# Kernel optimization log

Measured on AMD Instinct MI355X. Metric: run time of the kernel, lower is better.

## Reference

```python
import jax, jax.numpy as jnp
import numpy as np

T = 4      # num_step (also LSTM num_layers)
R = 64     # num_relation (= LSTM hidden size)
E = 1024   # num_entity
B = 128    # batch
IN = R + 2 * E  # LSTM input size


def _lstm_layer(x_seq, Wih, Whh, bih, bhh):
    # x_seq: [T, B, In]; torch gate order i, f, g, o
    Bsz = x_seq.shape[1]
    H = Whh.shape[1]
    pre = jnp.einsum('tbi,gi->tbg', x_seq, Wih) + bih + bhh  # [T,B,4H]

    def step(carry, z):
        h, c = carry
        z = z + h @ Whh.T
        i, f, g, o = jnp.split(z, 4, axis=-1)
        i, f, o = jax.nn.sigmoid(i), jax.nn.sigmoid(f), jax.nn.sigmoid(o)
        c = f * c + i * jnp.tanh(g)
        h = o * jnp.tanh(c)
        return (h, c), h

    init = (jnp.zeros((Bsz, H), x_seq.dtype), jnp.zeros((Bsz, H), x_seq.dtype))
    _, hs = jax.lax.scan(step, init, pre)
    return hs  # [T, B, H]


def setup_inputs() -> dict:
    key = jax.random.key(0)
    ks = jax.random.split(key, 12)
    s = 0.05
    inp = {
        'x': jax.random.uniform(ks[0], (B, IN), dtype=jnp.float32),
        'kb': jax.random.uniform(ks[1], (R, E, E), dtype=jnp.float32) * 0.01,
        # LSTM layer 0 (input dim IN)
        'Wih0': jax.random.normal(ks[2], (4 * R, IN), dtype=jnp.float32) * s,
        'Whh0': jax.random.normal(ks[3], (4 * R, R), dtype=jnp.float32) * s,
        'bih0': jnp.zeros((4 * R,), jnp.float32),
        'bhh0': jnp.zeros((4 * R,), jnp.float32),
        # LSTM layers 1..T-1 (input dim R)
        'Wih': jax.random.normal(ks[4], (T - 1, 4 * R, R), dtype=jnp.float32) * s,
        'Whh': jax.random.normal(ks[5], (T - 1, 4 * R, R), dtype=jnp.float32) * s,
        'bih': jnp.zeros((T - 1, 4 * R), jnp.float32),
        'bhh': jnp.zeros((T - 1, 4 * R), jnp.float32),
    }
    return inp


def reference(x, kb, Wih0, Whh0, bih0, bhh0, Wih, Whh, bih, bhh):
    # input to LSTM: x repeated T times -> [T, B, IN]
    seq = jnp.broadcast_to(x[None], (T,) + x.shape)
    hs = _lstm_layer(seq, Wih0, Whh0, bih0, bhh0)
    for l in range(T - 1):  # small fixed layer count
        hs = _lstm_layer(hs, Wih[l], Whh[l], bih[l], bhh[l])
    h = jax.nn.softmax(hs, axis=-1)  # [T, B, R] (first softmax)

    mem = [x[:, R:R + E]]  # memory[0] = head entity vector, [B, E]
    for i in range(T):
        h2 = jax.nn.softmax(h[i], axis=-1)  # double softmax, faithful to source
        # causal memory attention over steps k <= i
        att = jax.nn.softmax(jnp.einsum('kbr,br->bk', h[:i + 1], h[i]), axis=-1)  # [B, i+1]
        prev = jnp.einsum('bk,kbe->be', att, jnp.stack(mem))  # [B, E]
        # per-relation operator application: sum_r h2[b,r] * KB[r] @ prev[b]
        tmp = jnp.einsum('ref,bf->bre', kb, prev)  # [B, R, E]
        mem.append(jnp.einsum('br,bre->be', h2, tmp))

    tail = x[:, R + E:R + 2 * E]  # [B, E]
    score = jax.nn.sigmoid(-jnp.einsum('be,be->b', mem[-1], tail))[:, None]  # [B, 1]
    return score
```

## Files before the change

### kernel.cpp

```cpp
#include <hip/hip_runtime.h>
#include <cstdint>
#include <cstddef>

#define B_ 128
#define E_ 1024
#define R_ 64
#define T_ 4
#define IN_ 2112
#define G_ 256

typedef __attribute__((ext_vector_type(4))) float f32x4;
typedef __attribute__((ext_vector_type(8))) __bf16 bf16x8;

__device__ __forceinline__ unsigned short f2bf(float f) {
  unsigned int u = __float_as_uint(f);
  u += 0x7fffu + ((u >> 16) & 1u);
  return (unsigned short)(u >> 16);
}
__device__ __forceinline__ unsigned int pack2(float lo, float hi) {
  return (unsigned int)f2bf(lo) | ((unsigned int)f2bf(hi) << 16);
}
__device__ __forceinline__ float wred_sum(float v) {
#pragma unroll
  for (int m = 32; m > 0; m >>= 1) v += __shfl_xor(v, m, 64);
  return v;
}
__device__ __forceinline__ float wred_max(float v) {
#pragma unroll
  for (int m = 32; m > 0; m >>= 1) v = fmaxf(v, __shfl_xor(v, m, 64));
  return v;
}
__device__ __forceinline__ float sigmoidf_(float x) { return 1.f / (1.f + expf(-x)); }

__device__ __forceinline__ void gload_lds16(const void* g, void* l) {
  __builtin_amdgcn_global_load_lds(
      (const __attribute__((address_space(1))) unsigned int*)g,
      (__attribute__((address_space(3))) unsigned int*)l, 16, 0, 0);
}

__global__ __launch_bounds__(256) void head_kernel(
    const float* __restrict__ x, const float* __restrict__ kb,
    const float* __restrict__ Wih0, const float* __restrict__ Whh0,
    const float* __restrict__ bih0, const float* __restrict__ bhh0,
    const float* __restrict__ Wih, const float* __restrict__ Whh,
    const float* __restrict__ bih, const float* __restrict__ bhh,
    unsigned short* __restrict__ kb_bf,
    float* __restrict__ h2_out, float* __restrict__ att_out) {
  __shared__ float Wt[G_ * 65];
  __shared__ float xrow[IN_];
  __shared__ float hbuf[R_], cbuf[R_], zbuf[G_];
  __shared__ float hs_in[T_][R_], hs_out[T_][R_], hmat[T_][R_];
  const int tid = threadIdx.x;

  if (blockIdx.x >= 128) {
    const size_t base = (size_t)(blockIdx.x - 128) * 8192;
#pragma unroll
    for (int c = 0; c < 4; c++) {
      size_t o = base + (size_t)c * 2048 + (size_t)tid * 8;
      float4 v0 = *(const float4*)(kb + o);
      float4 v1 = *(const float4*)(kb + o + 4);
      uint4 u;
      u.x = pack2(v0.x, v0.y); u.y = pack2(v0.z, v0.w);
      u.z = pack2(v1.x, v1.y); u.w = pack2(v1.z, v1.w);
      *(uint4*)(kb_bf + o) = u;
    }
    return;
  }

  const int b = blockIdx.x;
  const int lane = tid & 63, wv = tid >> 6;

  for (int l = tid; l < IN_; l += 256) xrow[l] = x[b * IN_ + l];
  __syncthreads();
  float p0 = bih0[tid] + bhh0[tid];
  {
    const float* wr = Wih0 + (size_t)tid * IN_;
#pragma unroll 4
    for (int j = 0; j < IN_; j += 4) {
      float4 w = *(const float4*)(wr + j);
      p0 += xrow[j] * w.x + xrow[j + 1] * w.y + xrow[j + 2] * w.z + xrow[j + 3] * w.w;
    }
  }

  auto stage_w = [&](const float* src) {
    for (int l = tid; l < G_ * 16; l += 256) {
      int g = l >> 4, c4 = (l & 15) * 4;
      const float4 v = *(const float4*)(src + g * R_ + c4);
      float* dst = &Wt[g * 65 + c4];
      dst[0] = v.x; dst[1] = v.y; dst[2] = v.z; dst[3] = v.w;
    }
  };
  auto scan = [&](float* pret) {
    for (int t = 0; t < T_; t++) {
      float z = pret[t];
#pragma unroll
      for (int j = 0; j < R_; j++) z += hbuf[j] * Wt[tid * 65 + j];
      zbuf[tid] = z;
      __syncthreads();
      if (tid < R_) {
        float iv = sigmoidf_(zbuf[tid]);
        float fv = sigmoidf_(zbuf[R_ + tid]);
        float gv = tanhf(zbuf[2 * R_ + tid]);
        float ov = sigmoidf_(zbuf[3 * R_ + tid]);
        float c = fv * cbuf[tid] + iv * gv;
        cbuf[tid] = c;
        float h = ov * tanhf(c);
        hbuf[tid] = h;
        hs_out[t][tid] = h;
      }
      __syncthreads();
    }
  };

  float pret[T_];
#pragma unroll
  for (int t = 0; t < T_; t++) pret[t] = p0;
  stage_w(Whh0);
  if (tid < R_) { hbuf[tid] = 0.f; cbuf[tid] = 0.f; }
  __syncthreads();
  scan(pret);

  for (int l = 0; l < T_ - 1; l++) {
    hs_in[tid >> 6][tid & 63] = hs_out[tid >> 6][tid & 63];
    __syncthreads();
    stage_w(Wih + l * G_ * R_);
    __syncthreads();
    const float bsum = bih[l * G_ + tid] + bhh[l * G_ + tid];
    for (int t = 0; t < T_; t++) {
      float p = bsum;
#pragma unroll
      for (int j = 0; j < R_; j++) p += hs_in[t][j] * Wt[tid * 65 + j];
      pret[t] = p;
    }
    __syncthreads();
    stage_w(Whh + l * G_ * R_);
    if (tid < R_) { hbuf[tid] = 0.f; cbuf[tid] = 0.f; }
    __syncthreads();
    scan(pret);
  }

  {
    float v = hs_out[wv][lane];
    float mx = wred_max(v);
    float ev = expf(v - mx);
    float sm = wred_sum(ev);
    float hval = ev / sm;
    hmat[wv][lane] = hval;
    float mx2 = wred_max(hval);
    float e2 = expf(hval - mx2);
    float s2 = wred_sum(e2);
    h2_out[(wv * B_ + b) * R_ + lane] = e2 / s2;
    __syncthreads();
    float dots[T_];
    for (int k = 0; k <= wv; k++)
      dots[k] = wred_sum(hmat[k][lane] * hmat[wv][lane]);
    if (lane == 0) {
      float mx3 = dots[0];
      for (int k = 1; k <= wv; k++) mx3 = fmaxf(mx3, dots[k]);
      float ss = 0.f, es[T_];
      for (int k = 0; k <= wv; k++) { es[k] = expf(dots[k] - mx3); ss += es[k]; }
      for (int k = 0; k <= wv; k++) att_out[(wv * B_ + b) * 4 + k] = es[k] / ss;
    }
  }
}

__global__ __launch_bounds__(256) void prep0_kernel(
    const float* __restrict__ x, const float* __restrict__ att,
    unsigned short* __restrict__ prev_bf) {
  const int idx = blockIdx.x * 256 + threadIdx.x;
  const int b = idx >> 10, e = idx & 1023;
  float a0 = att[b * 4];
  prev_bf[idx] = f2bf(a0 * x[b * IN_ + R_ + e]);
}

__global__ __launch_bounds__(256) void gemm_bf_kernel(
    const unsigned short* __restrict__ Abf,
    const unsigned short* __restrict__ Kbf,
    float* __restrict__ part) {
  __shared__ unsigned short As[128 * 32];
  __shared__ unsigned short Bs[128 * 32];
  const int tid = threadIdx.x, wv = tid >> 6, lane = tid & 63;
  const int et = blockIdx.x, r = blockIdx.y;
  const int wm = (wv & 1) * 64, wn = (wv >> 1) * 64;
  const int fr = lane & 15, koff = (lane >> 4) * 8;

  const int srow = wv * 32 + (lane >> 2);
  const int scol = (lane & 3) * 8;
  const unsigned short* agp = Abf + (size_t)srow * 1024 + scol;
  const unsigned short* bgp = Kbf + (size_t)r * 1048576 + (size_t)(et * 128 + srow) * 1024 + scol;
  unsigned short* a_l0 = As + wv * 1024;
  unsigned short* a_l1 = As + wv * 1024 + 512;
  unsigned short* b_l0 = Bs + wv * 1024;
  unsigned short* b_l1 = Bs + wv * 1024 + 512;

  f32x4 acc[4][4];
#pragma unroll
  for (int mt = 0; mt < 4; mt++)
#pragma unroll
    for (int nt = 0; nt < 4; nt++)
#pragma unroll
      for (int q = 0; q < 4; q++) acc[mt][nt][q] = 0.f;

  for (int kk = 0; kk < 32; kk++) {
    gload_lds16(agp + kk * 32,             a_l0);
    gload_lds16(agp + kk * 32 + 16 * 1024, a_l1);
    gload_lds16(bgp + kk * 32,             b_l0);
    gload_lds16(bgp + kk * 32 + 16 * 1024, b_l1);
    __syncthreads();
    bf16x8 af[4], bfr[4];
#pragma unroll
    for (int mt = 0; mt < 4; mt++)
      af[mt] = *(const bf16x8*)(As + (wm + mt * 16 + fr) * 32 + koff);
#pragma unroll
    for (int nt = 0; nt < 4; nt++)
      bfr[nt] = *(const bf16x8*)(Bs + (wn + nt * 16 + fr) * 32 + koff);
#pragma unroll
    for (int mt = 0; mt < 4; mt++)
#pragma unroll
      for (int nt = 0; nt < 4; nt++)
        acc[mt][nt] = __builtin_amdgcn_mfma_f32_16x16x32_bf16(af[mt], bfr[nt], acc[mt][nt], 0, 0, 0);
    __syncthreads();
  }
  const int crow = (lane >> 4) * 4;
  float* pout = part + (size_t)r * 131072;
#pragma unroll
  for (int mt = 0; mt < 4; mt++)
#pragma unroll
    for (int nt = 0; nt < 4; nt++)
#pragma unroll
      for (int q = 0; q < 4; q++)
        pout[(wm + mt * 16 + crow + q) * 1024 + et * 128 + wn + nt * 16 + fr] = acc[mt][nt][q];
}

__global__ __launch_bounds__(256) void mid_kernel(
    const float* __restrict__ part, const float* __restrict__ h2,
    const float* __restrict__ att, const float* __restrict__ x,
    float* __restrict__ mem, unsigned short* __restrict__ prev_bf, int it) {
  const int idx = blockIdx.x * 256 + threadIdx.x;
  const int b = idx >> 10, e = idx & 1023;
  const float* h2row = h2 + (it * B_ + b) * R_;
  const float* pp = part + idx;
  float s = 0.f;
#pragma unroll 8
  for (int rr = 0; rr < 64; rr++) s += h2row[rr] * pp[(size_t)rr * 131072];
  mem[it * 131072 + idx] = s;
  if (it < 3) {
    const float* arow = att + ((it + 1) * B_ + b) * 4;
    float acc = arow[0] * x[b * IN_ + R_ + e];
    for (int k = 1; k <= it; k++) acc += arow[k] * mem[(k - 1) * 131072 + idx];
    acc += arow[it + 1] * s;
    prev_bf[idx] = f2bf(acc);
  }
}

__global__ __launch_bounds__(256) void prep_fp32_kernel(
    const float* __restrict__ x, const float* __restrict__ att,
    const float* __restrict__ mem, float* __restrict__ prev,
    float* __restrict__ newmem, int it) {
  const int idx = blockIdx.x * 256 + threadIdx.x;
  const int b = idx >> 10, e = idx & 1023;
  const float* arow = att + (it * B_ + b) * 4;
  float acc = arow[0] * x[b * IN_ + R_ + e];
  for (int k = 1; k <= it; k++)
    acc += arow[k] * mem[(k - 1) * (B_ * E_) + b * E_ + e];
  prev[idx] = acc;
  newmem[idx] = 0.f;
}

__global__ __launch_bounds__(256) void gemm_fp32_kernel(
    const float* __restrict__ prev, const float* __restrict__ h2,
    const float* __restrict__ kb, float* __restrict__ out) {
  __shared__ unsigned short As[128 * 40];
  __shared__ unsigned short Bs[128 * 40];
  __shared__ float h2s[128];
  const int tid = threadIdx.x;
  const int et = blockIdx.x;
  const int r = blockIdx.y;
  if (tid < 128) h2s[tid] = h2[tid * 64 + r];
  __syncthreads();
  const int row = tid >> 1;
  const int c0 = (tid & 1) * 16;
  const float hsc = h2s[row];
  const float* aptr = prev + row * 1024 + c0;
  const float* bptr = kb + (size_t)r * (1024u * 1024u) + (size_t)(et * 128 + row) * 1024 + c0;
  unsigned short* adst = As + row * 40 + c0;
  unsigned short* bdst = Bs + row * 40 + c0;
  const int wv = tid >> 6, lane = tid & 63;
  const int wm = (wv & 1) * 64, wn = (wv >> 1) * 64;
  const int fr = lane & 15, koff = (lane >> 4) * 8;
  f32x4 acc[4][4];
#pragma unroll
  for (int mt = 0; mt < 4; mt++)
#pragma unroll
    for (int nt = 0; nt < 4; nt++)
#pragma unroll
      for (int q = 0; q < 4; q++) acc[mt][nt][q] = 0.f;
  for (int kk = 0; kk < 32; kk++) {
    const float4 a0 = *(const float4*)(aptr + kk * 32);
    const float4 a1 = *(const float4*)(aptr + kk * 32 + 4);
    const float4 a2 = *(const float4*)(aptr + kk * 32 + 8);
    const float4 a3 = *(const float4*)(aptr + kk * 32 + 12);
    const float4 b0 = *(const float4*)(bptr + kk * 32);
    const float4 b1 = *(const float4*)(bptr + kk * 32 + 4);
    const float4 b2 = *(const float4*)(bptr + kk * 32 + 8);
    const float4 b3 = *(const float4*)(bptr + kk * 32 + 12);
    __syncthreads();
    uint4 u;
    u.x = pack2(a0.x * hsc, a0.y * hsc); u.y = pack2(a0.z * hsc, a0.w * hsc);
    u.z = pack2(a1.x * hsc, a1.y * hsc); u.w = pack2(a1.z * hsc, a1.w * hsc);
    *(uint4*)adst = u;
    u.x = pack2(a2.x * hsc, a2.y * hsc); u.y = pack2(a2.z * hsc, a2.w * hsc);
    u.z = pack2(a3.x * hsc, a3.y * hsc); u.w = pack2(a3.z * hsc, a3.w * hsc);
    *(uint4*)(adst + 8) = u;
    u.x = pack2(b0.x, b0.y); u.y = pack2(b0.z, b0.w);
    u.z = pack2(b1.x, b1.y); u.w = pack2(b1.z, b1.w);
    *(uint4*)bdst = u;
    u.x = pack2(b2.x, b2.y); u.y = pack2(b2.z, b2.w);
    u.z = pack2(b3.x, b3.y); u.w = pack2(b3.z, b3.w);
    *(uint4*)(bdst + 8) = u;
    __syncthreads();
    bf16x8 af[4], bfr[4];
#pragma unroll
    for (int mt = 0; mt < 4; mt++)
      af[mt] = *(const bf16x8*)(As + (wm + mt * 16 + fr) * 40 + koff);
#pragma unroll
    for (int nt = 0; nt < 4; nt++)
      bfr[nt] = *(const bf16x8*)(Bs + (wn + nt * 16 + fr) * 40 + koff);
#pragma unroll
    for (int mt = 0; mt < 4; mt++)
#pragma unroll
      for (int nt = 0; nt < 4; nt++)
        acc[mt][nt] = __builtin_amdgcn_mfma_f32_16x16x32_bf16(af[mt], bfr[nt], acc[mt][nt], 0, 0, 0);
  }
  const int crow = (lane >> 4) * 4;
  const int ccol = et * 128 + fr;
#pragma unroll
  for (int mt = 0; mt < 4; mt++)
#pragma unroll
    for (int nt = 0; nt < 4; nt++)
#pragma unroll
      for (int q = 0; q < 4; q++)
        atomicAdd(&out[(wm + mt * 16 + crow + q) * 1024 + ccol + wn + nt * 16], acc[mt][nt][q]);
}

__global__ __launch_bounds__(256) void score_kernel(
    const float* __restrict__ x, const float* __restrict__ mem4,
    float* __restrict__ out) {
  __shared__ float red[4];
  const int b = blockIdx.x, tid = threadIdx.x;
  float s = 0.f;
  for (int e = tid; e < E_; e += 256)
    s += mem4[b * E_ + e] * x[b * IN_ + R_ + E_ + e];
  s = wred_sum(s);
  if ((tid & 63) == 0) red[tid >> 6] = s;
  __syncthreads();
  if (tid == 0) {
    float t = red[0] + red[1] + red[2] + red[3];
    out[b] = 1.f / (1.f + expf(t));
  }
}

extern "C" void kernel_launch(void* const* d_in, const int* in_sizes, int n_in,
                              void* d_out, int out_size, void* d_ws, size_t ws_size,
                              hipStream_t stream) {
  const float* x    = (const float*)d_in[0];
  const float* kb   = (const float*)d_in[1];
  const float* Wih0 = (const float*)d_in[2];
  const float* Whh0 = (const float*)d_in[3];
  const float* bih0 = (const float*)d_in[4];
  const float* bhh0 = (const float*)d_in[5];
  const float* Wih  = (const float*)d_in[6];
  const float* Whh  = (const float*)d_in[7];
  const float* bih  = (const float*)d_in[8];
  const float* bhh  = (const float*)d_in[9];

  float* ws    = (float*)d_ws;
  float* h2    = ws;
  float* att   = ws + 32768;
  float* mem   = ws + 34816;
  float* prevb = ws + 559104;
  float* part  = ws + 690176;
  float* kbbf  = ws + 9078784;
  const size_t need_big = (size_t)(9078784 + 33554432) * sizeof(float);
  const bool big = ws_size >= need_big;

  if (big) {
    head_kernel<<<8320, 256, 0, stream>>>(x, kb, Wih0, Whh0, bih0, bhh0,
                                          Wih, Whh, bih, bhh,
                                          (unsigned short*)kbbf, h2, att);
    prep0_kernel<<<512, 256, 0, stream>>>(x, att, (unsigned short*)prevb);
    for (int i = 0; i < 4; i++) {
      gemm_bf_kernel<<<dim3(8, 64), 256, 0, stream>>>(
          (const unsigned short*)prevb, (const unsigned short*)kbbf, part);
      mid_kernel<<<512, 256, 0, stream>>>(part, h2, att, x, mem,
                                          (unsigned short*)prevb, i);
    }
  } else {
    head_kernel<<<128, 256, 0, stream>>>(x, kb, Wih0, Whh0, bih0, bhh0,
                                         Wih, Whh, bih, bhh,
                                         (unsigned short*)prevb , h2, att);
    for (int i = 0; i < 4; i++) {
      float* newmem = mem + i * (B_ * E_);
      prep_fp32_kernel<<<512, 256, 0, stream>>>(x, att, mem, prevb, newmem, i);
      gemm_fp32_kernel<<<dim3(8, 64), 256, 0, stream>>>(prevb, h2 + i * (B_ * R_), kb, newmem);
    }
  }
  score_kernel<<<128, 256, 0, stream>>>(x, mem + 3 * (B_ * E_), (float*)d_out);
}
```

Measured before the change: 602.8 us.

## Keep LSTM weights in registers, fuse prep0 into head, double-buffer GEMM

The head kernel's LSTM no longer stages weights through padded shared memory; each thread keeps its 64-wide weight row in registers. Gate math is done redundantly per wave with a double-buffered z array, which halves the barriers per step. The separate prep0 kernel is folded into head_kernel by writing the bf16 head-entity vector directly, relying on the step-0 attention being exactly 1. The bf16 MFMA GEMM now double-buffers its LDS tiles so the next K-slice loads while the current one computes, at the cost of twice the LDS and higher register pressure.

Result: slower. 620.8 us (+3.0%).

```diff
diff --git a/kernel.cpp b/kernel.cpp
--- a/kernel.cpp
+++ b/kernel.cpp
@@ -38,18 +38,15 @@
       (__attribute__((address_space(3))) unsigned int*)l, 16, 0, 0);
 }
 
-__global__ __launch_bounds__(256) void head_kernel(
+__global__ __launch_bounds__(256, 2) void head_kernel(
     const float* __restrict__ x, const float* __restrict__ kb,
     const float* __restrict__ Wih0, const float* __restrict__ Whh0,
     const float* __restrict__ bih0, const float* __restrict__ bhh0,
     const float* __restrict__ Wih, const float* __restrict__ Whh,
     const float* __restrict__ bih, const float* __restrict__ bhh,
     unsigned short* __restrict__ kb_bf,
-    float* __restrict__ h2_out, float* __restrict__ att_out) {
-  __shared__ float Wt[G_ * 65];
-  __shared__ float xrow[IN_];
-  __shared__ float hbuf[R_], cbuf[R_], zbuf[G_];
-  __shared__ float hs_in[T_][R_], hs_out[T_][R_], hmat[T_][R_];
+    float* __restrict__ h2_out, float* __restrict__ att_out,
+    unsigned short* __restrict__ prev_bf) {
   const int tid = threadIdx.x;
 
   if (blockIdx.x >= 128) {
@@ -67,76 +64,87 @@
     return;
   }
 
+  __shared__ __align__(16) float xrow[IN_];
+  __shared__ __align__(16) float hbuf[R_];
+  __shared__ __align__(16) float zbuf[2][G_];
+  __shared__ __align__(16) float hs_out[T_][R_];
+  __shared__ __align__(16) float hmat[T_][R_];
+
   const int b = blockIdx.x;
   const int lane = tid & 63, wv = tid >> 6;
+  const int s = tid & 63;
 
   for (int l = tid; l < IN_; l += 256) xrow[l] = x[b * IN_ + l];
   __syncthreads();
-  float p0 = bih0[tid] + bhh0[tid];
+  float p0;
   {
-    const float* wr = Wih0 + (size_t)tid * IN_;
-#pragma unroll 4
-    for (int j = 0; j < IN_; j += 4) {
-      float4 w = *(const float4*)(wr + j);
-      p0 += xrow[j] * w.x + xrow[j + 1] * w.y + xrow[j + 2] * w.z + xrow[j + 3] * w.w;
-    }
-  }
-
-  auto stage_w = [&](const float* src) {
-    for (int l = tid; l < G_ * 16; l += 256) {
-      int g = l >> 4, c4 = (l & 15) * 4;
-      const float4 v = *(const float4*)(src + g * R_ + c4);
-      float* dst = &Wt[g * 65 + c4];
-      dst[0] = v.x; dst[1] = v.y; dst[2] = v.z; dst[3] = v.w;
-    }
-  };
-  auto scan = [&](float* pret) {
+    float4 acc4 = {0.f, 0.f, 0.f, 0.f};
+    const float4* wr4 = (const float4*)(Wih0 + (size_t)tid * IN_);
+    const float4* xr4 = (const float4*)xrow;
+#pragma unroll 8
+    for (int j = 0; j < IN_ / 4; j++) {
+      float4 w = wr4[j];
+      float4 xv = xr4[j];
+      acc4.x += xv.x * w.x; acc4.y += xv.y * w.y;
+      acc4.z += xv.z * w.z; acc4.w += xv.w * w.w;
+    }
+    p0 = bih0[tid] + bhh0[tid] + ((acc4.x + acc4.y) + (acc4.z + acc4.w));
+  }
+
+  float4 w4[16];
+  float pret[T_];
+
+  auto scan = [&]() {
+    __syncthreads();
+    hbuf[s] = 0.f;
+    float creg = 0.f;
+#pragma unroll
     for (int t = 0; t < T_; t++) {
       float z = pret[t];
 #pragma unroll
-      for (int j = 0; j < R_; j++) z += hbuf[j] * Wt[tid * 65 + j];
-      zbuf[tid] = z;
+      for (int q = 0; q < 16; q++) {
+        float4 hv = *(const float4*)(&hbuf[q * 4]);
+        z += hv.x * w4[q].x + hv.y * w4[q].y + hv.z * w4[q].z + hv.w * w4[q].w;
+      }
+      zbuf[t & 1][tid] = z;
       __syncthreads();
-      if (tid < R_) {
-        float iv = sigmoidf_(zbuf[tid]);
-        float fv = sigmoidf_(zbuf[R_ + tid]);
-        float gv = tanhf(zbuf[2 * R_ + tid]);
-        float ov = sigmoidf_(zbuf[3 * R_ + tid]);
-        float c = fv * cbuf[tid] + iv * gv;
-        cbuf[tid] = c;
-        float h = ov * tanhf(c);
-        hbuf[tid] = h;
-        hs_out[t][tid] = h;
-      }
-      __syncthreads();
+      float iv = sigmoidf_(zbuf[t & 1][s]);
+      float fv = sigmoidf_(zbuf[t & 1][R_ + s]);
+      float gv = tanhf(zbuf[t & 1][2 * R_ + s]);
+      float ov = sigmoidf_(zbuf[t & 1][3 * R_ + s]);
+      creg = fv * creg + iv * gv;
+      float h = ov * tanhf(creg);
+      hbuf[s] = h;
+      hs_out[t][s] = h;
     }
   };
 
-  float pret[T_];
 #pragma unroll
   for (int t = 0; t < T_; t++) pret[t] = p0;
-  stage_w(Whh0);
-  if (tid < R_) { hbuf[tid] = 0.f; cbuf[tid] = 0.f; }
-  __syncthreads();
-  scan(pret);
+#pragma unroll
+  for (int q = 0; q < 16; q++)
+    w4[q] = *(const float4*)(Whh0 + (size_t)tid * R_ + q * 4);
+  scan();
 
   for (int l = 0; l < T_ - 1; l++) {
-    hs_in[tid >> 6][tid & 63] = hs_out[tid >> 6][tid & 63];
-    __syncthreads();
-    stage_w(Wih + l * G_ * R_);
-    __syncthreads();
+#pragma unroll
+    for (int q = 0; q < 16; q++)
+      w4[q] = *(const float4*)(Wih + ((size_t)l * G_ + tid) * R_ + q * 4);
     const float bsum = bih[l * G_ + tid] + bhh[l * G_ + tid];
+#pragma unroll
     for (int t = 0; t < T_; t++) {
       float p = bsum;
 #pragma unroll
-      for (int j = 0; j < R_; j++) p += hs_in[t][j] * Wt[tid * 65 + j];
+      for (int q = 0; q < 16; q++) {
+        float4 hv = *(const float4*)(&hs_out[t][q * 4]);
+        p += hv.x * w4[q].x + hv.y * w4[q].y + hv.z * w4[q].z + hv.w * w4[q].w;
+      }
       pret[t] = p;
     }
-    __syncthreads();
-    stage_w(Whh + l * G_ * R_);
-    if (tid < R_) { hbuf[tid] = 0.f; cbuf[tid] = 0.f; }
-    __syncthreads();
-    scan(pret);
+#pragma unroll
+    for (int q = 0; q < 16; q++)
+      w4[q] = *(const float4*)(Whh + ((size_t)l * G_ + tid) * R_ + q * 4);
+    scan();
   }
 
   {
@@ -162,23 +170,17 @@
       for (int k = 0; k <= wv; k++) att_out[(wv * B_ + b) * 4 + k] = es[k] / ss;
     }
   }
-}
-
-__global__ __launch_bounds__(256) void prep0_kernel(
-    const float* __restrict__ x, const float* __restrict__ att,
-    unsigned short* __restrict__ prev_bf) {
-  const int idx = blockIdx.x * 256 + threadIdx.x;
-  const int b = idx >> 10, e = idx & 1023;
-  float a0 = att[b * 4];
-  prev_bf[idx] = f2bf(a0 * x[b * IN_ + R_ + e]);
+
+  for (int l = tid; l < E_; l += 256)
+    prev_bf[b * E_ + l] = f2bf(xrow[R_ + l]);
 }
 
 __global__ __launch_bounds__(256) void gemm_bf_kernel(
     const unsigned short* __restrict__ Abf,
     const unsigned short* __restrict__ Kbf,
     float* __restrict__ part) {
-  __shared__ unsigned short As[128 * 32];
-  __shared__ unsigned short Bs[128 * 32];
+  __shared__ unsigned short As[2][128 * 32];
+  __shared__ unsigned short Bs[2][128 * 32];
   const int tid = threadIdx.x, wv = tid >> 6, lane = tid & 63;
   const int et = blockIdx.x, r = blockIdx.y;
   const int wm = (wv & 1) * 64, wn = (wv >> 1) * 64;
@@ -188,10 +190,6 @@
   const int scol = (lane & 3) * 8;
   const unsigned short* agp = Abf + (size_t)srow * 1024 + scol;
   const unsigned short* bgp = Kbf + (size_t)r * 1048576 + (size_t)(et * 128 + srow) * 1024 + scol;
-  unsigned short* a_l0 = As + wv * 1024;
-  unsigned short* a_l1 = As + wv * 1024 + 512;
-  unsigned short* b_l0 = Bs + wv * 1024;
-  unsigned short* b_l1 = Bs + wv * 1024 + 512;
 
   f32x4 acc[4][4];
 #pragma unroll
@@ -201,25 +199,32 @@
 #pragma unroll
       for (int q = 0; q < 4; q++) acc[mt][nt][q] = 0.f;
 
+  auto stage = [&](int buf, int kk) {
+    gload_lds16(agp + kk * 32,             As[buf] + wv * 1024);
+    gload_lds16(agp + kk * 32 + 16 * 1024, As[buf] + wv * 1024 + 512);
+    gload_lds16(bgp + kk * 32,             Bs[buf] + wv * 1024);
+    gload_lds16(bgp + kk * 32 + 16 * 1024, Bs[buf] + wv * 1024 + 512);
+  };
+
+  stage(0, 0);
+  __syncthreads();
+  int cur = 0;
   for (int kk = 0; kk < 32; kk++) {
-    gload_lds16(agp + kk * 32,             a_l0);
-    gload_lds16(agp + kk * 32 + 16 * 1024, a_l1);
-    gload_lds16(bgp + kk * 32,             b_l0);
-    gload_lds16(bgp + kk * 32 + 16 * 1024, b_l1);
-    __syncthreads();
+    if (kk < 31) stage(cur ^ 1, kk + 1);
     bf16x8 af[4], bfr[4];
 #pragma unroll
     for (int mt = 0; mt < 4; mt++)
-      af[mt] = *(const bf16x8*)(As + (wm + mt * 16 + fr) * 32 + koff);
-#pragma unroll
-    for (int nt = 0; nt < 4; nt++)
-      bfr[nt] = *(const bf16x8*)(Bs + (wn + nt * 16 + fr) * 32 + koff);
+      af[mt] = *(const bf16x8*)(As[cur] + (wm + mt * 16 + fr) * 32 + koff);
+#pragma unroll
+    for (int nt = 0; nt < 4; nt++)
+      bfr[nt] = *(const bf16x8*)(Bs[cur] + (wn + nt * 16 + fr) * 32 + koff);
 #pragma unroll
     for (int mt = 0; mt < 4; mt++)
 #pragma unroll
       for (int nt = 0; nt < 4; nt++)
         acc[mt][nt] = __builtin_amdgcn_mfma_f32_16x16x32_bf16(af[mt], bfr[nt], acc[mt][nt], 0, 0, 0);
     __syncthreads();
+    cur ^= 1;
   }
   const int crow = (lane >> 4) * 4;
   float* pout = part + (size_t)r * 131072;
@@ -387,8 +392,8 @@
   if (big) {
     head_kernel<<<8320, 256, 0, stream>>>(x, kb, Wih0, Whh0, bih0, bhh0,
                                           Wih, Whh, bih, bhh,
-                                          (unsigned short*)kbbf, h2, att);
-    prep0_kernel<<<512, 256, 0, stream>>>(x, att, (unsigned short*)prevb);
+                                          (unsigned short*)kbbf, h2, att,
+                                          (unsigned short*)prevb);
     for (int i = 0; i < 4; i++) {
       gemm_bf_kernel<<<dim3(8, 64), 256, 0, stream>>>(
           (const unsigned short*)prevb, (const unsigned short*)kbbf, part);
@@ -398,7 +403,8 @@
   } else {
     head_kernel<<<128, 256, 0, stream>>>(x, kb, Wih0, Whh0, bih0, bhh0,
                                          Wih, Whh, bih, bhh,
-                                         (unsigned short*)prevb , h2, att);
+                                         (unsigned short*)prevb , h2, att,
+                                         (unsigned short*)prevb);
     for (int i = 0; i < 4; i++) {
       float* newmem = mem + i * (B_ * E_);
       prep_fp32_kernel<<<512, 256, 0, stream>>>(x, att, mem, prevb, newmem, i);
```
